# Kernel tuning notes

Measured on AMD Instinct MI355X. Metric: run time of the kernel, lower is better.

The kernel has to match this reference:

```python
import jax, jax.numpy as jnp
import numpy as np

B, F, D = 4096, 39, 16          # batch, num_field, embedding_size
V = 1000000                     # num_feat (vocab)
H1, H2 = 128, 128               # cin_layer_sizes
INPUT_DIM = F * D               # 624
FC_DIM = H1 // 2 + H2           # 192 (split_half)
DEEP = [400, 400]
BN_EPS = 1e-5


def setup_inputs() -> dict:
    key = jax.random.key(0)
    ks = jax.random.split(key, 16)
    xav = lambda k, shp: jax.random.normal(k, shp, jnp.float32) * np.sqrt(2.0 / (shp[0] + shp[-1]))
    return {
        "feat_index": jax.random.randint(ks[0], (B, F), 0, V),
        "feat_value": jax.random.uniform(ks[1], (B, F), jnp.float32),
        "emb_table": xav(ks[2], (V, D)),
        "linear_w": xav(ks[3], (INPUT_DIM, 1)),
        "linear_b": jnp.zeros((1,), jnp.float32),
        "conv_w1": xav(ks[4], (H1, F, F)),          # (out, h_prev, m) == conv1d 1x1 weight reshaped
        "conv_b1": jnp.zeros((H1,), jnp.float32),
        "conv_w2": xav(ks[5], (H2, H1 // 2, F)),
        "conv_b2": jnp.zeros((H2,), jnp.float32),
        "deep_w1": xav(ks[6], (INPUT_DIM, DEEP[0])),
        "deep_b1": jnp.zeros((DEEP[0],), jnp.float32),
        "bn_g1": jnp.ones((DEEP[0],), jnp.float32),
        "bn_b1": jnp.zeros((DEEP[0],), jnp.float32),
        "deep_w2": xav(ks[7], (DEEP[0], DEEP[1])),
        "deep_b2": jnp.zeros((DEEP[1],), jnp.float32),
        "bn_g2": jnp.ones((DEEP[1],), jnp.float32),
        "bn_b2": jnpp if False else jnp.zeros((DEEP[1],), jnp.float32),
        "out_w": xav(ks[8], (1 + FC_DIM + DEEP[1], 1)),
        "out_b": jnp.zeros((1,), jnp.float32),
    }


def _bn(x, g, b):
    # torch BatchNorm1d in training mode: biased batch variance
    m = x.mean(axis=0)
    v = x.var(axis=0)
    return g * (x - m) * jax.lax.rsqrt(v + BN_EPS) + b


def reference(feat_index, feat_value, emb_table, linear_w, linear_b,
              conv_w1, conv_b1, conv_w2, conv_b2,
              deep_w1, deep_b1, bn_g1, bn_b1,
              deep_w2, deep_b2, bn_g2, bn_b2,
              out_w, out_b):
    e = emb_table[feat_index]                      # [B, F, D]
    flat = e.reshape(e.shape[0], -1)               # [B, F*D]
    linear_part = flat @ linear_w + linear_b       # [B, 1]

    # CIN: fused outer-product + 1x1 conv (x_k[b,o,d] = sum_{h,m} W[o,h,m] x_prev[b,h,d] x0[b,m,d])
    x0 = e
    h1 = jax.nn.relu(jnp.einsum('bhd,bmd,ohm->bod', x0, x0, conv_w1) + conv_b1[None, :, None])
    nxt, hi1 = jnp.split(h1, 2, axis=1)            # split_half
    h2 = jax.nn.relu(jnp.einsum('bhd,bmd,ohm->bod', nxt, x0, conv_w2) + conv_b2[None, :, None])
    res = jnp.concatenate([hi1, h2], axis=1).sum(axis=2)   # [B, FC_DIM]

    # Deep tower (dropout off / deterministic)
    y = jax.nn.relu(_bn(flat @ deep_w1 + deep_b1, bn_g1, bn_b1))
    y = jax.nn.relu(_bn(y @ deep_w2 + deep_b2, bn_g2, bn_b2))

    cat = jnp.concatenate([linear_part, res, y], axis=1)   # [B, 593]
    return cat @ out_w + out_b
```

## Files before the change

### kernel.cpp

```cpp
#include <hip/hip_runtime.h>

#define BATCH   4096
#define NF      39
#define ED      16
#define IN_DIM  624
#define DW      400
#define BN_EPS  1e-5f
#define NKSG    80
#define AK1     640
#define NKS1    20
#define NKS2    13
#define WCOL    416

typedef __attribute__((ext_vector_type(8))) short short8;
typedef __attribute__((ext_vector_type(4))) float f32x4;
typedef unsigned short u16;

__device__ inline unsigned pack_hi2(float a, float b) {
  return __builtin_amdgcn_perm(__float_as_uint(b), __float_as_uint(a), 0x07060302u);
}
__device__ inline unsigned bf16_rne(float f) {
  unsigned u = __float_as_uint(f);
  u += 0x7fff + ((u >> 16) & 1);
  return u >> 16;
}
__device__ inline float bf2f(u16 v) { return __uint_as_float((unsigned)v << 16); }

#define CIN_E (NKSG * 128 * 32)
#define D1_E  (NKS1 * WCOL * 32)
#define D2_E  (NKS2 * WCOL * 32)
#define PREP_E (CIN_E + D1_E + D2_E + 1600)
#define PREP_B ((PREP_E + 255) / 256)

__global__ __launch_bounds__(256) void k_gp(const int* __restrict__ idx,
    const float* __restrict__ emb, const float* __restrict__ lw,
    const float* __restrict__ lb, const float* __restrict__ w1,
    const float* __restrict__ w2, const float* __restrict__ dw1,
    const float* __restrict__ dw2, u16* __restrict__ flatb,
    float* __restrict__ lp, u16* __restrict__ wp1, u16* __restrict__ wp2,
    u16* __restrict__ wpd1, u16* __restrict__ wpd2, float* __restrict__ gstat) {
  int t = threadIdx.x;
  if (blockIdx.x < BATCH) {
    int b = blockIdx.x;
    __shared__ int si[NF];
    __shared__ float r4[4];
    if (t < NF) si[t] = idx[b * NF + t];
    __syncthreads();
    float acc = 0.f;
#pragma unroll
    for (int i = 0; i < 3; i++) {
      int e = t + i * 256;
      if (e < IN_DIM) {
        float v = emb[(size_t)si[e >> 4] * ED + (e & 15)];
        flatb[(size_t)b * AK1 + e] = (u16)bf16_rne(v);
        acc = fmaf(v, lw[e], acc);
      } else if (e < AK1) {
        flatb[(size_t)b * AK1 + e] = 0;
      }
    }
#pragma unroll
    for (int k = 1; k < 64; k <<= 1) acc += __shfl_xor(acc, k);
    if ((t & 63) == 0) r4[t >> 6] = acc;
    __syncthreads();
    if (t == 0) lp[b] = r4[0] + r4[1] + r4[2] + r4[3] + lb[0];
  } else {
    int e = (blockIdx.x - BATCH) * 256 + t;
    if (e < CIN_E) {
      int ksg = e >> 12, r = e & 4095, n = r >> 5, kk = r & 31;
      int k = ksg * 32 + kk, h = k & 63, m = k >> 6;
      float v1 = (h < NF && m < NF) ? w1[(size_t)n * (NF * NF) + h * NF + m] : 0.f;
      float v2 = (m < NF) ? w2[(size_t)n * (64 * NF) + h * NF + m] : 0.f;
      wp1[e] = (u16)bf16_rne(v1);
      wp2[e] = (u16)bf16_rne(v2);
    } else if (e < CIN_E + D1_E) {
      int e2 = e - CIN_E;
      int ksg = e2 / (WCOL * 32), r = e2 - ksg * (WCOL * 32);
      int col = r >> 5, kk = r & 31;
      int k = ksg * 32 + kk;
      wpd1[e2] = (k < IN_DIM && col < DW) ? (u16)bf16_rne(dw1[(size_t)k * DW + col]) : 0;
    } else if (e < CIN_E + D1_E + D2_E) {
      int e2 = e - CIN_E - D1_E;
      int ksg = e2 / (WCOL * 32), r = e2 - ksg * (WCOL * 32);
      int col = r >> 5, kk = r & 31;
      int k = ksg * 32 + kk;
      wpd2[e2] = (k < DW && col < DW) ? (u16)bf16_rne(dw2[(size_t)k * DW + col]) : 0;
    } else if (e < PREP_E) {
      gstat[e - CIN_E - D1_E - D2_E] = 0.f;
    }
  }
}

template <bool LAY2>
__global__ __launch_bounds__(256, 2) void k_cin_mfma(
    const u16* __restrict__ flatb, const u16* __restrict__ nxtg,
    const u16* __restrict__ wp, const float* __restrict__ bias,
    u16* __restrict__ nxt_out, float* __restrict__ res) {
  __shared__ f32x4 lds4[2 * 16 * 64];
  int t = threadIdx.x;
  int w = t >> 6, lane = t & 63;
  int pair = w >> 1, half = w & 1;
  int nl = lane & 15, q = lane >> 4;
  int d = nl;
  int b0 = blockIdx.x * 8 + pair * 4;
  int c0 = blockIdx.y * 64;
  int M0 = half * 20;

  unsigned nxr[4][2][4];
  if (LAY2) {
#pragma unroll
    for (int si = 0; si < 4; si++)
#pragma unroll
      for (int ks = 0; ks < 2; ks++) {
        uint4 v = *(const uint4*)(nxtg +
            (((size_t)(b0 + si) * 16 + d) * 64 + ks * 32 + q * 8));
        nxr[si][ks][0] = v.x; nxr[si][ks][1] = v.y;
        nxr[si][ks][2] = v.z; nxr[si][ks][3] = v.w;
      }
  } else {
#pragma unroll
    for (int si = 0; si < 4; si++)
#pragma unroll
      for (int ks = 0; ks < 2; ks++)
#pragma unroll
        for (int w4 = 0; w4 < 4; w4++) {
          int h0 = ks * 32 + q * 8 + 2 * w4;
          int h1 = h0 + 1;
          unsigned u0 = (h0 < NF) ? flatb[(size_t)(b0 + si) * AK1 + h0 * 16 + d] : 0;
          unsigned u1 = (h1 < NF) ? flatb[(size_t)(b0 + si) * AK1 + h1 * 16 + d] : 0;
          nxr[si][ks][w4] = u0 | (u1 << 16);
        }
  }

  f32x4 acc[4][4];
#pragma unroll
  for (int si = 0; si < 4; si++)
#pragma unroll
    for (int nt = 0; nt < 4; nt++) acc[si][nt] = (f32x4){0.f, 0.f, 0.f, 0.f};

  const u16* wbase = wp + (size_t)(c0 + nl) * 32 + q * 8;
  short8 bfr[2][4];
#pragma unroll
  for (int nt = 0; nt < 4; nt++)
    bfr[0][nt] = *(const short8*)(wbase + (size_t)(M0 * 2) * 4096 + nt * 512);

  float xv[4], xvn[4];
#pragma unroll
  for (int si = 0; si < 4; si++)
    xv[si] = bf2f(flatb[(size_t)(b0 + si) * AK1 + M0 * 16 + d]);

#pragma unroll 2
  for (int i = 0; i < 20; i++) {
    int m = M0 + i;
    if (i + 1 < 20) {
#pragma unroll
      for (int si = 0; si < 4; si++)
        xvn[si] = bf2f(flatb[(size_t)(b0 + si) * AK1 + (m + 1) * 16 + d]);
    }
#pragma unroll
    for (int ks = 0; ks < 2; ks++) {
      int nx = ks ^ 1;
      int nksg = m * 2 + ks + 1;
      if (ks == 0 || i + 1 < 20) {
        const u16* wb = wbase + (size_t)nksg * 4096;
#pragma unroll
        for (int nt = 0; nt < 4; nt++)
          bfr[nx][nt] = *(const short8*)(wb + nt * 512);
      }
      short8 afr[4];
#pragma unroll
      for (int si = 0; si < 4; si++) {
        union { unsigned u[4]; short8 s; } a;
#pragma unroll
        for (int w4 = 0; w4 < 4; w4++) {
          unsigned u = nxr[si][ks][w4];
          float lo = __uint_as_float(u << 16) * xv[si];
          float hi = __uint_as_float(u & 0xffff0000u) * xv[si];
          a.u[w4] = pack_hi2(lo, hi);
        }
        afr[si] = a.s;
      }
#pragma unroll
      for (int nt = 0; nt < 4; nt++)
#pragma unroll
        for (int si = 0; si < 4; si++)
          acc[si][nt] = __builtin_amdgcn_mfma_f32_16x16x32_bf16(
              afr[si], bfr[ks][nt], acc[si][nt], 0, 0, 0);
    }
#pragma unroll
    for (int si = 0; si < 4; si++) xv[si] = xvn[si];
  }

  if (half) {
#pragma unroll
    for (int si = 0; si < 4; si++)
#pragma unroll
      for (int nt = 0; nt < 4; nt++)
        lds4[(pair * 16 + si * 4 + nt) * 64 + lane] = acc[si][nt];
  }
  __syncthreads();
  if (half) return;
#pragma unroll
  for (int si = 0; si < 4; si++)
#pragma unroll
    for (int nt = 0; nt < 4; nt++) {
      f32x4 p = lds4[(pair * 16 + si * 4 + nt) * 64 + lane];
      acc[si][nt][0] += p[0]; acc[si][nt][1] += p[1];
      acc[si][nt][2] += p[2]; acc[si][nt][3] += p[3];
    }

#pragma unroll
  for (int si = 0; si < 4; si++) {
    int b = b0 + si;
#pragma unroll
    for (int nt = 0; nt < 4; nt++) {
      int o = c0 + nt * 16 + nl;
      float bi = bias[o];
      if (!LAY2 && c0 == 0) {
#pragma unroll
        for (int r = 0; r < 4; r++) {
          float v = fmaxf(acc[si][nt][r] + bi, 0.f);
          nxt_out[((size_t)b * 16 + q * 4 + r) * 64 + o] = (u16)bf16_rne(v);
        }
      } else {
        float s = 0.f;
#pragma unroll
        for (int r = 0; r < 4; r++) s += fmaxf(acc[si][nt][r] + bi, 0.f);
        s += __shfl_xor(s, 16);
        s += __shfl_xor(s, 32);
        if (q == 0) {
          int ri = LAY2 ? (64 + o) : (o - 64);
          res[(size_t)b * 192 + ri] = s;
        }
      }
    }
  }
}

template <bool BN_A, int NKS, int KREAL, int AK>
__global__ __launch_bounds__(256) void k_gemm_mfma(
    const u16* __restrict__ Abf, const float* __restrict__ Af32,
    const u16* __restrict__ wp, const float* __restrict__ bias,
    const float* __restrict__ gsIn, const float* __restrict__ gs2In,
    const float* __restrict__ bng, const float* __restrict__ bnb,
    float* __restrict__ C, float* __restrict__ gs, float* __restrict__ gs2) {
  __shared__ float lsS[NKS * 32], lsH[NKS * 32];
  __shared__ float lred[64];
  int t = threadIdx.x;
  if (BN_A) {
    for (int c = t; c < NKS * 32; c += 256) {
      float sc = 0.f, sh = 0.f;
      if (c < DW) {
        float m = gsIn[c] * (1.f / BATCH);
        float var = gs2In[c] * (1.f / BATCH) - m * m;
        sc = bng[c] * rsqrtf(var + BN_EPS);
        sh = bnb[c] - m * sc;
      }
      lsS[c] = sc; lsH[c] = sh;
    }
  }
  if (t < 64) lred[t] = 0.f;
  __syncthreads();

  int w = t >> 6, lane = t & 63;
  int nl = lane & 15, q = lane >> 4;
  int row = blockIdx.x * 64 + w * 16 + nl;
  int c0 = blockIdx.y * 32;
  f32x4 acc[2];
  acc[0] = (f32x4){0.f, 0.f, 0.f, 0.f};
  acc[1] = (f32x4){0.f, 0.f, 0.f, 0.f};

  short8 araw[2]; f32x4 fraw0[2], fraw1[2]; short8 braw[2][2];
  auto loadA_raw = [&](int ksg, int buf) {
    int kb = ksg * 32 + q * 8;
    if (!BN_A) {
      araw[buf] = *(const short8*)(Abf + (size_t)row * AK + kb);
    } else {
      if (kb + 8 <= KREAL) {
        fraw0[buf] = *(const f32x4*)(Af32 + (size_t)row * KREAL + kb);
        fraw1[buf] = *(const f32x4*)(Af32 + (size_t)row * KREAL + kb + 4);
      } else {
        fraw0[buf] = (f32x4){0.f,0.f,0.f,0.f};
        fraw1[buf] = (f32x4){0.f,0.f,0.f,0.f};
      }
    }
    const u16* wb = wp + (size_t)ksg * (WCOL * 32) + (size_t)(c0 + nl) * 32 + q * 8;
    braw[buf][0] = *(const short8*)wb;
    braw[buf][1] = *(const short8*)(wb + 16 * 32);
  };
  auto cookA = [&](int ksg, int buf) -> short8 {
    if (!BN_A) return araw[buf];
    int kb = ksg * 32 + q * 8;
    f32x4 s0 = *(const f32x4*)&lsS[kb], h0 = *(const f32x4*)&lsH[kb];
    f32x4 s1 = *(const f32x4*)&lsS[kb + 4], h1 = *(const f32x4*)&lsH[kb + 4];
    union { unsigned u[4]; short8 s; } a;
    float v0 = fmaxf(fmaf(fraw0[buf][0], s0[0], h0[0]), 0.f);
    float v1 = fmaxf(fmaf(fraw0[buf][1], s0[1], h0[1]), 0.f);
    float v2 = fmaxf(fmaf(fraw0[buf][2], s0[2], h0[2]), 0.f);
    float v3 = fmaxf(fmaf(fraw0[buf][3], s0[3], h0[3]), 0.f);
    float v4 = fmaxf(fmaf(fraw1[buf][0], s1[0], h1[0]), 0.f);
    float v5 = fmaxf(fmaf(fraw1[buf][1], s1[1], h1[1]), 0.f);
    float v6 = fmaxf(fmaf(fraw1[buf][2], s1[2], h1[2]), 0.f);
    float v7 = fmaxf(fmaf(fraw1[buf][3], s1[3], h1[3]), 0.f);
    a.u[0] = bf16_rne(v0) | (bf16_rne(v1) << 16);
    a.u[1] = bf16_rne(v2) | (bf16_rne(v3) << 16);
    a.u[2] = bf16_rne(v4) | (bf16_rne(v5) << 16);
    a.u[3] = bf16_rne(v6) | (bf16_rne(v7) << 16);
    return a.s;
  };

  loadA_raw(0, 0);
#pragma unroll 4
  for (int ksg = 0; ksg < NKS; ksg++) {
    int cur = ksg & 1;
    if (ksg + 1 < NKS) loadA_raw(ksg + 1, cur ^ 1);
    short8 afr = cookA(ksg, cur);
    acc[0] = __builtin_amdgcn_mfma_f32_16x16x32_bf16(afr, braw[cur][0], acc[0], 0, 0, 0);
    acc[1] = __builtin_amdgcn_mfma_f32_16x16x32_bf16(afr, braw[cur][1], acc[1], 0, 0, 0);
  }

  int rbase = blockIdx.x * 64 + w * 16 + q * 4;
#pragma unroll
  for (int nt = 0; nt < 2; nt++) {
    int col = c0 + nt * 16 + nl;
    if (col < DW) {
      float bi = bias[col];
      float s = 0.f, s2 = 0.f;
#pragma unroll
      for (int r = 0; r < 4; r++) {
        float v = acc[nt][r] + bi;
        C[(size_t)(rbase + r) * DW + col] = v;
        s += v; s2 = fmaf(v, v, s2);
      }
      s += __shfl_xor(s, 16); s2 += __shfl_xor(s2, 16);
      s += __shfl_xor(s, 32); s2 += __shfl_xor(s2, 32);
      if (q == 0) {
        atomicAdd(&lred[nt * 16 + nl], s);
        atomicAdd(&lred[32 + nt * 16 + nl], s2);
      }
    }
  }
  __syncthreads();
  if (t < 32) {
    int col = c0 + t;
    if (col < DW) atomicAdd(&gs[col], lred[t]);
  } else if (t < 64) {
    int col = c0 + t - 32;
    if (col < DW) atomicAdd(&gs2[col], lred[t]);
  }
}

__global__ __launch_bounds__(256) void k_final(const float* __restrict__ lp,
    const float* __restrict__ res, const float* __restrict__ y2,
    const float* __restrict__ gB, const float* __restrict__ gB2,
    const float* __restrict__ g2, const float* __restrict__ bb2,
    const float* __restrict__ ow, const float* __restrict__ ob,
    float* __restrict__ out) {
  __shared__ float lsS[DW], lsH[DW];
  int t = threadIdx.x;
  for (int c = t; c < DW; c += 256) {
    float m = gB[c] * (1.f / BATCH);
    float var = gB2[c] * (1.f / BATCH) - m * m;
    float sc = g2[c] * rsqrtf(var + BN_EPS);
    lsS[c] = sc;
    lsH[c] = bb2[c] - m * sc;
  }
  __syncthreads();
  int lane = t & 63, w = t >> 6;
  int b = blockIdx.x * 4 + w;
  float acc = 0.f;
  for (int j = lane; j < 593; j += 64) {
    float v;
    if (j == 0)       v = lp[b];
    else if (j < 193) v = res[(size_t)b * 192 + (j - 1)];
    else {
      int c = j - 193;
      v = fmaxf(fmaf(y2[(size_t)b * DW + c], lsS[c], lsH[c]), 0.f);
    }
    acc = fmaf(v, ow[j], acc);
  }
#pragma unroll
  for (int k = 1; k < 64; k <<= 1) acc += __shfl_xor(acc, k);
  if (lane == 0) out[b] = acc + ob[0];
}

extern "C" void kernel_launch(void* const* d_in, const int* in_sizes, int n_in,
                              void* d_out, int out_size, void* d_ws, size_t ws_size,
                              hipStream_t stream) {
  const int*   feat_index = (const int*)d_in[0];
  const float* emb = (const float*)d_in[2];
  const float* lw  = (const float*)d_in[3];
  const float* lb  = (const float*)d_in[4];
  const float* w1  = (const float*)d_in[5];
  const float* b1  = (const float*)d_in[6];
  const float* w2  = (const float*)d_in[7];
  const float* b2  = (const float*)d_in[8];
  const float* dw1 = (const float*)d_in[9];
  const float* db1 = (const float*)d_in[10];
  const float* g1  = (const float*)d_in[11];
  const float* bb1 = (const float*)d_in[12];
  const float* dw2 = (const float*)d_in[13];
  const float* db2 = (const float*)d_in[14];
  const float* g2  = (const float*)d_in[15];
  const float* bb2 = (const float*)d_in[16];
  const float* ow  = (const float*)d_in[17];
  const float* ob  = (const float*)d_in[18];

  float* ws   = (float*)d_ws;
  u16*  flatb = (u16*)ws;
  float* y1   = ws + 1310720;
  float* res  = ws + 2949120;
  float* lp   = ws + 3735552;
  float* gA   = ws + 3741248;
  float* gA2  = gA + 400;
  float* gB   = gA2 + 400;
  float* gB2  = gB + 400;
  u16*  nxtg  = (u16*)(ws + 3742848);
  float* y2   = ws + 3742848;
  u16*  wp1   = (u16*)(ws + 5840000);
  u16*  wp2   = (u16*)(ws + 6003840);
  u16*  wpd1  = (u16*)(ws + 6167680);
  u16*  wpd2  = (u16*)(ws + 6300800);
  float* out  = (float*)d_out;

  k_gp<<<BATCH + PREP_B, 256, 0, stream>>>(feat_index, emb, lw, lb, w1, w2,
      dw1, dw2, flatb, lp, wp1, wp2, wpd1, wpd2, gA);
  k_cin_mfma<false><<<dim3(BATCH / 8, 2), 256, 0, stream>>>(
      flatb, nullptr, wp1, b1, nxtg, res);
  k_cin_mfma<true><<<dim3(BATCH / 8, 2), 256, 0, stream>>>(
      flatb, nxtg, wp2, b2, nullptr, res);
  k_gemm_mfma<false, NKS1, IN_DIM, AK1><<<dim3(BATCH / 64, 13), 256, 0, stream>>>(
      flatb, nullptr, wpd1, db1, nullptr, nullptr, nullptr, nullptr, y1, gA, gA2);
  k_gemm_mfma<true, NKS2, DW, 0><<<dim3(BATCH / 64, 13), 256, 0, stream>>>(
      nullptr, y1, wpd2, db2, gA, gA2, g1, bb1, y2, gB, gB2);
  k_final<<<BATCH / 4, 256, 0, stream>>>(lp, res, y2, gB, gB2, g2, bb2, ow, ob, out);
}
```

Baseline: 287.2 us.

## Restructure CIN kernel to full-K per wave with triple-buffered weights

The CIN MFMA kernel no longer splits the m-range across two waves and reduces through LDS. Each wave now covers the whole 39-field range for its own 4 batch rows, so a block handles 16 batches and the grid halves. Weight fragments are triple-buffered, and the CIN weight packing is trimmed to 78 k-groups so the padded m slice is skipped. The gather kernel is also changed to one wave per batch row, broadcasting indices with shuffles instead of LDS and block syncs, and the A-operand scaling uses packed f32x2 multiplies. The cost is a longer serial K loop per wave and fewer blocks in flight.

```diff
diff --git a/kernel.cpp b/kernel.cpp
--- a/kernel.cpp
+++ b/kernel.cpp
@@ -6,7 +6,7 @@
 #define IN_DIM  624
 #define DW      400
 #define BN_EPS  1e-5f
-#define NKSG    80
+#define NKSG    78
 #define AK1     640
 #define NKS1    20
 #define NKS2    13
@@ -14,6 +14,7 @@
 
 typedef __attribute__((ext_vector_type(8))) short short8;
 typedef __attribute__((ext_vector_type(4))) float f32x4;
+typedef __attribute__((ext_vector_type(2))) float f32x2;
 typedef unsigned short u16;
 
 __device__ inline unsigned pack_hi2(float a, float b) {
@@ -31,6 +32,7 @@
 #define D2_E  (NKS2 * WCOL * 32)
 #define PREP_E (CIN_E + D1_E + D2_E + 1600)
 #define PREP_B ((PREP_E + 255) / 256)
+#define GATH_B (BATCH / 4)
 
 __global__ __launch_bounds__(256) void k_gp(const int* __restrict__ idx,
     const float* __restrict__ emb, const float* __restrict__ lw,
@@ -40,36 +42,34 @@
     float* __restrict__ lp, u16* __restrict__ wp1, u16* __restrict__ wp2,
     u16* __restrict__ wpd1, u16* __restrict__ wpd2, float* __restrict__ gstat) {
   int t = threadIdx.x;
-  if (blockIdx.x < BATCH) {
-    int b = blockIdx.x;
-    __shared__ int si[NF];
-    __shared__ float r4[4];
-    if (t < NF) si[t] = idx[b * NF + t];
-    __syncthreads();
+  if (blockIdx.x < GATH_B) {
+    int lane = t & 63;
+    int b = blockIdx.x * 4 + (t >> 6);
+    int sj = (lane < NF) ? idx[b * NF + lane] : 0;
     float acc = 0.f;
 #pragma unroll
-    for (int i = 0; i < 3; i++) {
-      int e = t + i * 256;
+    for (int i = 0; i < 10; i++) {
+      int e = lane + i * 64;
       if (e < IN_DIM) {
-        float v = emb[(size_t)si[e >> 4] * ED + (e & 15)];
+        int f = e >> 4;
+        int row = __shfl(sj, f);
+        float v = emb[(size_t)row * ED + (e & 15)];
         flatb[(size_t)b * AK1 + e] = (u16)bf16_rne(v);
         acc = fmaf(v, lw[e], acc);
-      } else if (e < AK1) {
+      } else {
         flatb[(size_t)b * AK1 + e] = 0;
       }
     }
 #pragma unroll
     for (int k = 1; k < 64; k <<= 1) acc += __shfl_xor(acc, k);
-    if ((t & 63) == 0) r4[t >> 6] = acc;
-    __syncthreads();
-    if (t == 0) lp[b] = r4[0] + r4[1] + r4[2] + r4[3] + lb[0];
+    if (lane == 0) lp[b] = acc + lb[0];
   } else {
-    int e = (blockIdx.x - BATCH) * 256 + t;
+    int e = (blockIdx.x - GATH_B) * 256 + t;
     if (e < CIN_E) {
       int ksg = e >> 12, r = e & 4095, n = r >> 5, kk = r & 31;
       int k = ksg * 32 + kk, h = k & 63, m = k >> 6;
-      float v1 = (h < NF && m < NF) ? w1[(size_t)n * (NF * NF) + h * NF + m] : 0.f;
-      float v2 = (m < NF) ? w2[(size_t)n * (64 * NF) + h * NF + m] : 0.f;
+      float v1 = (h < NF) ? w1[(size_t)n * (NF * NF) + h * NF + m] : 0.f;
+      float v2 = w2[(size_t)n * (64 * NF) + h * NF + m];
       wp1[e] = (u16)bf16_rne(v1);
       wp2[e] = (u16)bf16_rne(v2);
     } else if (e < CIN_E + D1_E) {
@@ -95,17 +95,14 @@
     const u16* __restrict__ flatb, const u16* __restrict__ nxtg,
     const u16* __restrict__ wp, const float* __restrict__ bias,
     u16* __restrict__ nxt_out, float* __restrict__ res) {
-  __shared__ f32x4 lds4[2 * 16 * 64];
   int t = threadIdx.x;
   int w = t >> 6, lane = t & 63;
-  int pair = w >> 1, half = w & 1;
   int nl = lane & 15, q = lane >> 4;
   int d = nl;
-  int b0 = blockIdx.x * 8 + pair * 4;
+  int b0 = blockIdx.x * 16 + w * 4;
   int c0 = blockIdx.y * 64;
-  int M0 = half * 20;
-
-  unsigned nxr[4][2][4];
+
+  f32x2 nxf[4][2][4];
   if (LAY2) {
 #pragma unroll
     for (int si = 0; si < 4; si++)
@@ -113,8 +110,11 @@
       for (int ks = 0; ks < 2; ks++) {
         uint4 v = *(const uint4*)(nxtg +
             (((size_t)(b0 + si) * 16 + d) * 64 + ks * 32 + q * 8));
-        nxr[si][ks][0] = v.x; nxr[si][ks][1] = v.y;
-        nxr[si][ks][2] = v.z; nxr[si][ks][3] = v.w;
+        unsigned uu[4] = {v.x, v.y, v.z, v.w};
+#pragma unroll
+        for (int w4 = 0; w4 < 4; w4++)
+          nxf[si][ks][w4] = (f32x2){__uint_as_float(uu[w4] << 16),
+                                    __uint_as_float(uu[w4] & 0xffff0000u)};
       }
   } else {
 #pragma unroll
@@ -125,9 +125,9 @@
         for (int w4 = 0; w4 < 4; w4++) {
           int h0 = ks * 32 + q * 8 + 2 * w4;
           int h1 = h0 + 1;
-          unsigned u0 = (h0 < NF) ? flatb[(size_t)(b0 + si) * AK1 + h0 * 16 + d] : 0;
-          unsigned u1 = (h1 < NF) ? flatb[(size_t)(b0 + si) * AK1 + h1 * 16 + d] : 0;
-          nxr[si][ks][w4] = u0 | (u1 << 16);
+          float f0 = (h0 < NF) ? bf2f(flatb[(size_t)(b0 + si) * AK1 + h0 * 16 + d]) : 0.f;
+          float f1 = (h1 < NF) ? bf2f(flatb[(size_t)(b0 + si) * AK1 + h1 * 16 + d]) : 0.f;
+          nxf[si][ks][w4] = (f32x2){f0, f1};
         }
   }
 
@@ -138,44 +138,44 @@
     for (int nt = 0; nt < 4; nt++) acc[si][nt] = (f32x4){0.f, 0.f, 0.f, 0.f};
 
   const u16* wbase = wp + (size_t)(c0 + nl) * 32 + q * 8;
-  short8 bfr[2][4];
-#pragma unroll
-  for (int nt = 0; nt < 4; nt++)
-    bfr[0][nt] = *(const short8*)(wbase + (size_t)(M0 * 2) * 4096 + nt * 512);
+  short8 bfr[3][4];
+#pragma unroll
+  for (int nt = 0; nt < 4; nt++) {
+    bfr[0][nt] = *(const short8*)(wbase + nt * 512);
+    bfr[1][nt] = *(const short8*)(wbase + 4096 + nt * 512);
+  }
 
   float xv[4], xvn[4];
 #pragma unroll
   for (int si = 0; si < 4; si++)
-    xv[si] = bf2f(flatb[(size_t)(b0 + si) * AK1 + M0 * 16 + d]);
-
-#pragma unroll 2
-  for (int i = 0; i < 20; i++) {
-    int m = M0 + i;
-    if (i + 1 < 20) {
-#pragma unroll
-      for (int si = 0; si < 4; si++)
-        xvn[si] = bf2f(flatb[(size_t)(b0 + si) * AK1 + (m + 1) * 16 + d]);
-    }
-#pragma unroll
-    for (int ks = 0; ks < 2; ks++) {
-      int nx = ks ^ 1;
-      int nksg = m * 2 + ks + 1;
-      if (ks == 0 || i + 1 < 20) {
-        const u16* wb = wbase + (size_t)nksg * 4096;
+    xv[si] = bf2f(flatb[(size_t)(b0 + si) * AK1 + d]);
+
+  for (int mg = 0; mg < 13; mg++) {
+#pragma unroll
+    for (int j = 0; j < 6; j++) {
+      int ksg = mg * 6 + j;
+      int ks = j & 1;
+      if (j < 4 || mg < 12) {
+        const u16* wb = wbase + (size_t)(ksg + 2) * 4096;
 #pragma unroll
         for (int nt = 0; nt < 4; nt++)
-          bfr[nx][nt] = *(const short8*)(wb + nt * 512);
+          bfr[(j + 2) % 3][nt] = *(const short8*)(wb + nt * 512);
+      }
+      if (ks == 0) {
+        int m = ksg >> 1;
+#pragma unroll
+        for (int si = 0; si < 4; si++)
+          xvn[si] = bf2f(flatb[(size_t)(b0 + si) * AK1 + (m + 1) * 16 + d]);
       }
       short8 afr[4];
 #pragma unroll
       for (int si = 0; si < 4; si++) {
         union { unsigned u[4]; short8 s; } a;
+        f32x2 xv2 = (f32x2){xv[si], xv[si]};
 #pragma unroll
         for (int w4 = 0; w4 < 4; w4++) {
-          unsigned u = nxr[si][ks][w4];
-          float lo = __uint_as_float(u << 16) * xv[si];
-          float hi = __uint_as_float(u & 0xffff0000u) * xv[si];
-          a.u[w4] = pack_hi2(lo, hi);
+          f32x2 p = nxf[si][ks][w4] * xv2;
+          a.u[w4] = pack_hi2(p[0], p[1]);
         }
         afr[si] = a.s;
       }
@@ -184,29 +184,13 @@
 #pragma unroll
         for (int si = 0; si < 4; si++)
           acc[si][nt] = __builtin_amdgcn_mfma_f32_16x16x32_bf16(
-              afr[si], bfr[ks][nt], acc[si][nt], 0, 0, 0);
-    }
-#pragma unroll
-    for (int si = 0; si < 4; si++) xv[si] = xvn[si];
-  }
-
-  if (half) {
-#pragma unroll
-    for (int si = 0; si < 4; si++)
-#pragma unroll
-      for (int nt = 0; nt < 4; nt++)
-        lds4[(pair * 16 + si * 4 + nt) * 64 + lane] = acc[si][nt];
-  }
-  __syncthreads();
-  if (half) return;
-#pragma unroll
-  for (int si = 0; si < 4; si++)
-#pragma unroll
-    for (int nt = 0; nt < 4; nt++) {
-      f32x4 p = lds4[(pair * 16 + si * 4 + nt) * 64 + lane];
-      acc[si][nt][0] += p[0]; acc[si][nt][1] += p[1];
-      acc[si][nt][2] += p[2]; acc[si][nt][3] += p[3];
-    }
+              afr[si], bfr[j % 3][nt], acc[si][nt], 0, 0, 0);
+      if (ks == 1) {
+#pragma unroll
+        for (int si = 0; si < 4; si++) xv[si] = xvn[si];
+      }
+    }
+  }
 
 #pragma unroll
   for (int si = 0; si < 4; si++) {
@@ -422,11 +406,11 @@
   u16*  wpd2  = (u16*)(ws + 6300800);
   float* out  = (float*)d_out;
 
-  k_gp<<<BATCH + PREP_B, 256, 0, stream>>>(feat_index, emb, lw, lb, w1, w2,
+  k_gp<<<GATH_B + PREP_B, 256, 0, stream>>>(feat_index, emb, lw, lb, w1, w2,
       dw1, dw2, flatb, lp, wp1, wp2, wpd1, wpd2, gA);
-  k_cin_mfma<false><<<dim3(BATCH / 8, 2), 256, 0, stream>>>(
+  k_cin_mfma<false><<<dim3(BATCH / 16, 2), 256, 0, stream>>>(
       flatb, nullptr, wp1, b1, nxtg, res);
-  k_cin_mfma<true><<<dim3(BATCH / 8, 2), 256, 0, stream>>>(
+  k_cin_mfma<true><<<dim3(BATCH / 16, 2), 256, 0, stream>>>(
       flatb, nxtg, wp2, b2, nullptr, res);
   k_gemm_mfma<false, NKS1, IN_DIM, AK1><<<dim3(BATCH / 64, 13), 256, 0, stream>>>(
       flatb, nullptr, wpd1, db1, nullptr, nullptr, nullptr, nullptr, y1, gA, gA2);
```

Result: faster. 270.6 us (-5.8%).
